# Kernel tuning notes

Hardware: AMD Instinct MI355X
Metric: run time of the kernel (lower is better)

Reference implementation:

```python
import jax, jax.numpy as jnp
import numpy as np


def setup_inputs() -> dict:
    key = jax.random.key(0)
    k_q, k_k, k_v, k_xd, k_yd = jax.random.split(key, 5)
    B, L, H, E, K = 8, 4096, 2048, 512, 64
    return {
        "queries": jax.random.normal(k_q, (B, L, E), dtype=jnp.float32),
        "keys": jax.random.normal(k_k, (B, L, E), dtype=jnp.float32),
        "values": jax.random.normal(k_v, (B, L, E), dtype=jnp.float32),
        "x_date": jax.random.normal(k_xd, (B, L, K), dtype=jnp.float32),
        "y_date": jax.random.normal(k_yd, (B, H, K), dtype=jnp.float32),
    }


def reference(queries, keys, values, x_date, y_date):
    # queries/keys are unused in the original forward's math (only shapes).
    k = x_date.shape[-1]
    scale = 1.0 / float(np.sqrt(k))  # self.scale is None -> 1/sqrt(k)
    # scores: [B, L, H] from date features
    scores = jnp.einsum('blk,bhk->blh', x_date, y_date)
    # softmax over target axis H (dim=-1), numerically stable
    A = jax.nn.softmax(scale * scores, axis=-1)  # [B, L, H]
    # weighted reduction over source axis L -> [B, H, E]
    V = jnp.einsum('ble,blh->bhe', values, A)
    return V
```

## Files before the change

### kernel.cpp

```cpp
#include <hip/hip_runtime.h>
#include <hip/hip_bf16.h>

#define BN 8
#define LN 4096
#define HN 2048
#define EN 512
#define KN 64
#define LT 32
#define NIT 128

typedef __attribute__((ext_vector_type(8))) short bf16x8;
typedef __attribute__((ext_vector_type(4))) float f32x4;
typedef __attribute__((ext_vector_type(4))) unsigned u32x4;

__device__ __forceinline__ short f2b(float x) {
  union { float f; unsigned u; } v; v.f = x;
  unsigned r = v.u + 0x7fffu + ((v.u >> 16) & 1u);
  return (short)(r >> 16);
}

__device__ __forceinline__ bf16x8 cvt8(const float* __restrict__ p) {
  f32x4 a = *(const f32x4*)(p);
  f32x4 b = *(const f32x4*)(p + 4);
  bf16x8 r;
  r[0] = f2b(a[0]); r[1] = f2b(a[1]); r[2] = f2b(a[2]); r[3] = f2b(a[3]);
  r[4] = f2b(b[0]); r[5] = f2b(b[1]); r[6] = f2b(b[2]); r[7] = f2b(b[3]);
  return r;
}

__device__ __forceinline__ void gload16(const void* g, void* s) {
  __builtin_amdgcn_global_load_lds(
      (const __attribute__((address_space(1))) unsigned int*)(unsigned long long)g,
      (__attribute__((address_space(3))) unsigned int*)(unsigned int)(unsigned long long)s,
      16, 0, 0);
}

__global__ __launch_bounds__(256) void prep_cvt2(const float* __restrict__ xs,
                                                 short* __restrict__ xo,
                                                 const float* __restrict__ ys,
                                                 short* __restrict__ yo) {
  int bx = blockIdx.x;
  const float* src;
  short* dst;
  float scale;
  int i;
  if (bx < 1024) {
    i = bx * 256 + threadIdx.x;
    src = xs; dst = xo; scale = 0.125f * 1.4426950408889634f;
  } else {
    i = (bx - 1024) * 256 + threadIdx.x;
    src = ys; dst = yo; scale = 1.0f;
  }
  f32x4 a = *(const f32x4*)(src + (size_t)i * 8);
  f32x4 b = *(const f32x4*)(src + (size_t)i * 8 + 4);
  bf16x8 r;
  r[0] = f2b(a[0] * scale); r[1] = f2b(a[1] * scale);
  r[2] = f2b(a[2] * scale); r[3] = f2b(a[3] * scale);
  r[4] = f2b(b[0] * scale); r[5] = f2b(b[1] * scale);
  r[6] = f2b(b[2] * scale); r[7] = f2b(b[3] * scale);
  *(bf16x8*)(dst + (size_t)i * 8) = r;
}

__global__ __launch_bounds__(256) void k_pv_stats(const float* __restrict__ vals,
                                                  short* __restrict__ valsT,
                                                  const short* __restrict__ xb,
                                                  const short* __restrict__ yb,
                                                  float* __restrict__ ps) {
  __shared__ unsigned trT[2048];
  const int bx = blockIdx.x;
  const int tid = threadIdx.x;
  if (bx < 4096) {
    const int b = bx >> 9;
    const int e0 = ((bx >> 6) & 7) * 64;
    const int l0 = (bx & 63) * 64;
    {
      int lr2 = tid >> 3;
      int ec = (tid & 7) * 8;
      const float* r0 = vals + ((size_t)b * LN + l0 + 2 * lr2) * EN + e0 + ec;
      const float* r1 = r0 + EN;
      f32x4 a0 = *(const f32x4*)r0, a1 = *(const f32x4*)(r0 + 4);
      f32x4 c0 = *(const f32x4*)r1, c1 = *(const f32x4*)(r1 + 4);
#pragma unroll
      for (int j = 0; j < 8; ++j) {
        float lo = (j < 4) ? a0[j] : a1[j - 4];
        float hi = (j < 4) ? c0[j] : c1[j - 4];
        unsigned dw = (unsigned)(unsigned short)f2b(lo) |
                      ((unsigned)(unsigned short)f2b(hi) << 16);
        int e = ec + j;
        int sz = (((e >> 3) ^ e) & 7) << 2;
        trT[e * 32 + (lr2 ^ sz)] = dw;
      }
    }
    __syncthreads();
    {
      int er = tid >> 2, lq = (tid & 3) * 8;
      int sr = ((er >> 3) ^ er) & 7;
      const unsigned* base = trT + er * 32;
      u32x4 u0 = *(const u32x4*)(base + ((((lq >> 2) + 0) ^ sr) << 2));
      u32x4 u1 = *(const u32x4*)(base + ((((lq >> 2) + 1) ^ sr) << 2));
      short* dst = valsT + ((size_t)b * EN + e0 + er) * LN + l0 + 2 * lq;
      *(u32x4*)dst = u0;
      *(u32x4*)(dst + 8) = u1;
    }
  } else {
    const int idx = bx - 4096;
    const int b = (idx >> 5) & 7, hc = idx >> 8;
    const int w = tid >> 6, lane = tid & 63;
    const int row = lane & 15, g = lane >> 4;
    const int lb = (idx & 31) * 128 + w * 32;
    const size_t bL = (size_t)b * LN, bH = (size_t)b * HN;
    bf16x8 xa[2][2];
#pragma unroll
    for (int lt = 0; lt < 2; ++lt) {
      const short* xp = xb + ((bL + lb + lt * 16 + row) << 6) + 8 * g;
      xa[lt][0] = *(const bf16x8*)xp;
      xa[lt][1] = *(const bf16x8*)(xp + 32);
    }
    float s[2][4] = {{0.f, 0.f, 0.f, 0.f}, {0.f, 0.f, 0.f, 0.f}};
    const short* ybase = yb + ((bH + hc * 512 + row) << 6) + 8 * g;
#pragma unroll 2
    for (int it = 0; it < 32; ++it) {
      const short* yp = ybase + ((size_t)it << 10);
      bf16x8 y0 = *(const bf16x8*)yp;
      bf16x8 y1 = *(const bf16x8*)(yp + 32);
#pragma unroll
      for (int lt = 0; lt < 2; ++lt) {
        f32x4 a = {0.f, 0.f, 0.f, 0.f};
        a = __builtin_amdgcn_mfma_f32_16x16x32_bf16(xa[lt][0], y0, a, 0, 0, 0);
        a = __builtin_amdgcn_mfma_f32_16x16x32_bf16(xa[lt][1], y1, a, 0, 0, 0);
#pragma unroll
        for (int r = 0; r < 4; ++r) s[lt][r] += __builtin_amdgcn_exp2f(a[r]);
      }
    }
#pragma unroll
    for (int d = 1; d < 16; d <<= 1)
#pragma unroll
      for (int lt = 0; lt < 2; ++lt)
#pragma unroll
        for (int r = 0; r < 4; ++r) s[lt][r] += __shfl_xor(s[lt][r], d);
    if (row == 0) {
#pragma unroll
      for (int lt = 0; lt < 2; ++lt)
#pragma unroll
        for (int r = 0; r < 4; ++r)
          ps[(size_t)hc * (BN * LN) + bL + lb + lt * 16 + 4 * g + r] = s[lt][r];
    }
  }
}

__global__ void k_comb(const float* __restrict__ ps, float* __restrict__ wv) {
  int idx = blockIdx.x * 256 + threadIdx.x;
  float z = ps[idx] + ps[BN * LN + idx] + ps[2 * BN * LN + idx] + ps[3 * BN * LN + idx];
  wv[idx] = 1.0f / z;
}

__global__ __launch_bounds__(512, 4) void k_main4(
    const short* __restrict__ valsT, const short* __restrict__ xb,
    const short* __restrict__ yb, const float* __restrict__ wv,
    float* __restrict__ out) {
  __shared__ __align__(16) char smem[70016];
  const int tid = threadIdx.x;
  const int w = tid >> 6, lane = tid & 63;
  const int row = lane & 15, g = lane >> 4;

  const int f = blockIdx.x;
  const int b = f & 7;
  const int rest = f >> 3;
  const int hb = (rest & 31) * 64;
  const int eb = (rest >> 5) * 256;
  const size_t bL = (size_t)b * LN, bH = (size_t)b * HN;

  const int wbase = __builtin_amdgcn_readfirstlane(tid & ~63);

  const short* vsrc[2];
#pragma unroll
  for (int j = 0; j < 2; ++j) {
    int i = j * 512 + tid;
    int e = i >> 2, sl = (i & 3) ^ ((e >> 1) & 3);
    vsrc[j] = valsT + (((size_t)b * EN + eb + e) << 12) + 8 * sl;
  }
  const short* xsrc;
  {
    int p = w * 32 + (lane & 31);
    int l = p >> 3, sl = (p & 7) ^ (l & 7);
    xsrc = xb + ((bL + l) << 6) + 8 * sl;
  }
  const float* ssrc = wv + bL + 4 * tid;

  auto stage = [&](int buf, int tl) {
    int loff = tl * 32;
    if (lane < 32)
      gload16(xsrc + loff * 64, smem + 49152 + buf * 4096 + wbase * 8);
    if (tid < 8)
      gload16(ssrc + loff, smem + 69632 + buf * 128);
#pragma unroll
    for (int j = 0; j < 2; ++j)
      gload16(vsrc[j] + loff, smem + buf * 16384 + (j * 8192 + wbase * 16));
  };

  const int ht = w >> 1, lt = w & 1;
  bf16x8 ya0, ya1;
  {
    const short* yp = yb + ((bH + hb + ht * 16 + row) << 6) + 8 * g;
    ya0 = *(const bf16x8*)yp;
    ya1 = *(const bf16x8*)(yp + 32);
  }
  const int sp0 = g ^ (row & 7);
  const int xoffA = ((lt * 16 + row) << 7) + (sp0 << 4);
  const int xoffB = ((lt * 16 + row) << 7) + ((sp0 ^ 4) << 4);
  const int swoff = (lt * 16 + 4 * g) * 4;
  const int hq1 = ht * 16 + row;
  const int poff_w = hq1 * 64 + (((2 * lt + (g >> 1)) ^ ((hq1 >> 1) & 3)) << 4) + (g & 1) * 8;
  const int hq2a = (w >> 2) * 32 + row, hq2b = hq2a + 16;
  const int paoffA = hq2a * 64 + ((g ^ ((hq2a >> 1) & 3)) << 4);
  const int paoffB = hq2b * 64 + ((g ^ ((hq2b >> 1) & 3)) << 4);
  int vboff[4];
#pragma unroll
  for (int n = 0; n < 4; ++n) {
    int el = (w & 3) * 64 + n * 16 + row;
    vboff[n] = el * 64 + ((g ^ ((el >> 1) & 3)) << 4);
  }

  f32x4 acc[2][4];
#pragma unroll
  for (int at = 0; at < 2; ++at)
#pragma unroll
    for (int n = 0; n < 4; ++n) acc[at][n] = (f32x4){0.f, 0.f, 0.f, 0.f};

  auto produce = [&](int bx1, int pp) {
    const char* xbuf = smem + 49152 + bx1 * 4096;
    bf16x8 xa0 = *(const bf16x8*)(xbuf + xoffA);
    bf16x8 xa1 = *(const bf16x8*)(xbuf + xoffB);
    f32x4 sws = *(const f32x4*)(smem + 69632 + bx1 * 128 + swoff);
    f32x4 s4 = {0.f, 0.f, 0.f, 0.f};
    s4 = __builtin_amdgcn_mfma_f32_16x16x32_bf16(xa0, ya0, s4, 0, 0, 0);
    s4 = __builtin_amdgcn_mfma_f32_16x16x32_bf16(xa1, ya1, s4, 0, 0, 0);
    unsigned u0 = (unsigned)(unsigned short)f2b(__builtin_amdgcn_exp2f(s4[0]) * sws[0]) |
                  ((unsigned)(unsigned short)f2b(__builtin_amdgcn_exp2f(s4[1]) * sws[1]) << 16);
    unsigned u1 = (unsigned)(unsigned short)f2b(__builtin_amdgcn_exp2f(s4[2]) * sws[2]) |
                  ((unsigned)(unsigned short)f2b(__builtin_amdgcn_exp2f(s4[3]) * sws[3]) << 16);
    *(unsigned long long*)(smem + 61440 + pp * 4096 + poff_w) =
        (unsigned long long)u0 | ((unsigned long long)u1 << 32);
  };

  auto consume = [&](int rbv, int pp) {
    const char* vbuf = smem + rbv * 16384;
    const char* pbuf = smem + 61440 + pp * 4096;
    bf16x8 pa0 = *(const bf16x8*)(pbuf + paoffA);
    bf16x8 pa1 = *(const bf16x8*)(pbuf + paoffB);
    __builtin_amdgcn_s_setprio(1);
#pragma unroll
    for (int n = 0; n < 4; ++n) {
      bf16x8 vb = *(const bf16x8*)(vbuf + vboff[n]);
      acc[0][n] = __builtin_amdgcn_mfma_f32_16x16x32_bf16(pa0, vb, acc[0][n], 0, 0, 0);
      acc[1][n] = __builtin_amdgcn_mfma_f32_16x16x32_bf16(pa1, vb, acc[1][n], 0, 0, 0);
    }
    __builtin_amdgcn_s_setprio(0);
  };

  stage(0, 0);
  stage(1, 1);
  asm volatile("s_waitcnt vmcnt(2)" ::: "memory");
  __builtin_amdgcn_s_barrier();
  produce(0, 0);
  asm volatile("s_waitcnt lgkmcnt(0)" ::: "memory");
  __builtin_amdgcn_s_barrier();

  int rbv = 0, bx1 = 1, sb = 2, p = 0;
  for (int it = 0; it < NIT - 1; ++it) {
    if (it < NIT - 2) stage(sb, it + 2);
    produce(bx1, p ^ 1);
    consume(rbv, p);
    if (it < NIT - 2)
      asm volatile("s_waitcnt vmcnt(2) lgkmcnt(0)" ::: "memory");
    else
      asm volatile("s_waitcnt vmcnt(0) lgkmcnt(0)" ::: "memory");
    __builtin_amdgcn_s_barrier();
    rbv = rbv == 2 ? 0 : rbv + 1;
    bx1 = bx1 == 2 ? 0 : bx1 + 1;
    sb = sb == 2 ? 0 : sb + 1;
    p ^= 1;
  }
  consume(rbv, p);

#pragma unroll
  for (int at = 0; at < 2; ++at)
#pragma unroll
    for (int n = 0; n < 4; ++n)
#pragma unroll
      for (int r = 0; r < 4; ++r) {
        int h = hb + (w >> 2) * 32 + at * 16 + 4 * g + r;
        int e = eb + (w & 3) * 64 + n * 16 + row;
        out[(bH + h) * (size_t)EN + e] = acc[at][n][r];
      }
}

__global__ __launch_bounds__(256) void k_stats_o(const float* __restrict__ xd,
                                                 const float* __restrict__ yd,
                                                 float* __restrict__ mz) {
  const int b = blockIdx.y;
  const int w = threadIdx.x >> 6;
  const int lane = threadIdx.x & 63;
  const int row = lane & 15, g = lane >> 4;
  const int lb = blockIdx.x * 64 + w * 16;
  const float* xp = xd + ((size_t)b * LN + lb + row) * KN + g * 8;
  bf16x8 a0 = cvt8(xp), a1 = cvt8(xp + 32);
  float m[4], s[4];
#pragma unroll
  for (int r = 0; r < 4; ++r) { m[r] = -1e30f; s[r] = 0.f; }
  const float* ybp = yd + ((size_t)b * HN + row) * KN + g * 8;
  for (int h0 = 0; h0 < HN; h0 += 16) {
    bf16x8 b0 = cvt8(ybp + (size_t)h0 * KN);
    bf16x8 b1 = cvt8(ybp + (size_t)h0 * KN + 32);
    f32x4 acc = {0.f, 0.f, 0.f, 0.f};
    acc = __builtin_amdgcn_mfma_f32_16x16x32_bf16(a0, b0, acc, 0, 0, 0);
    acc = __builtin_amdgcn_mfma_f32_16x16x32_bf16(a1, b1, acc, 0, 0, 0);
#pragma unroll
    for (int r = 0; r < 4; ++r) {
      float v = acc[r] * 0.125f;
      float mn = fmaxf(m[r], v);
      s[r] = s[r] * __expf(m[r] - mn) + __expf(v - mn);
      m[r] = mn;
    }
  }
#pragma unroll
  for (int d = 1; d < 16; d <<= 1) {
#pragma unroll
    for (int r = 0; r < 4; ++r) {
      float mo = __shfl_xor(m[r], d);
      float so = __shfl_xor(s[r], d);
      float mn = fmaxf(m[r], mo);
      s[r] = s[r] * __expf(m[r] - mn) + so * __expf(mo - mn);
      m[r] = mn;
    }
  }
  if (row == 0) {
#pragma unroll
    for (int r = 0; r < 4; ++r) {
      size_t idx = (size_t)b * LN + lb + 4 * g + r;
      mz[idx] = m[r];
      mz[(size_t)BN * LN + idx] = 1.0f / s[r];
    }
  }
}

__global__ __launch_bounds__(512) void k_main_o(const float* __restrict__ vals,
                                                const float* __restrict__ xd,
                                                const float* __restrict__ yd,
                                                const float* __restrict__ mz,
                                                float* __restrict__ out) {
  __shared__ short vT[256][34];
  __shared__ short pT[128][34];
  __shared__ short xT[LT][72];
  __shared__ float smm[LT], smz[LT];
  const int b = blockIdx.z;
  const int hb = blockIdx.x * 128;
  const int eb = blockIdx.y * 256;
  const int tid = threadIdx.x;
  const int w = tid >> 6, lane = tid & 63;
  const int row = lane & 15, g = lane >> 4;
  const float* yp = yd + ((size_t)b * HN + hb + w * 16 + row) * KN + g * 8;
  bf16x8 ya0 = cvt8(yp), ya1 = cvt8(yp + 32);
  f32x4 acc[16];
#pragma unroll
  for (int n = 0; n < 16; ++n) acc[n] = (f32x4){0.f, 0.f, 0.f, 0.f};
  const float* mzb = mz + (size_t)b * LN;
  const float* rzb = mz + (size_t)BN * LN + (size_t)b * LN;
  for (int l0 = 0; l0 < LN; l0 += LT) {
    __syncthreads();
    {
      int xl = tid >> 4, xk = (tid & 15) * 4;
      f32x4 xv = *(const f32x4*)(xd + ((size_t)b * LN + l0 + xl) * KN + xk);
      union { short h[4]; int i[2]; } u;
      u.h[0] = f2b(xv[0]); u.h[1] = f2b(xv[1]); u.h[2] = f2b(xv[2]); u.h[3] = f2b(xv[3]);
      int* dst = (int*)(&xT[xl][xk]);
      dst[0] = u.i[0]; dst[1] = u.i[1];
    }
#pragma unroll
    for (int lp = 0; lp < 4; ++lp) {
      int vl = (tid >> 6) + lp * 8;
      const float* vrow = vals + ((size_t)b * LN + l0 + vl) * EN + eb;
#pragma unroll
      for (int u2 = 0; u2 < 4; ++u2) {
        int e = (tid & 63) + u2 * 64;
        vT[e][vl] = f2b(vrow[e]);
      }
    }
    if (tid < LT) { smm[tid] = mzb[l0 + tid]; smz[tid] = rzb[l0 + tid]; }
    __syncthreads();
#pragma unroll
    for (int t2 = 0; t2 < 2; ++t2) {
      const short* xr = &xT[t2 * 16 + row][0];
      bf16x8 xb0 = *(const bf16x8*)(xr + 8 * g);
      bf16x8 xb1 = *(const bf16x8*)(xr + 32 + 8 * g);
      f32x4 sa = {0.f, 0.f, 0.f, 0.f};
      sa = __builtin_amdgcn_mfma_f32_16x16x32_bf16(ya0, xb0, sa, 0, 0, 0);
      sa = __builtin_amdgcn_mfma_f32_16x16x32_bf16(ya1, xb1, sa, 0, 0, 0);
      int lcol = t2 * 16 + row;
      float mm = smm[lcol], zz = smz[lcol];
#pragma unroll
      for (int r = 0; r < 4; ++r) {
        float p2 = __expf(sa[r] * 0.125f - mm) * zz;
        pT[w * 16 + 4 * g + r][lcol] = f2b(p2);
      }
    }
    __syncthreads();
    bf16x8 pa;
    {
      const int* pi = (const int*)(&pT[w * 16 + row][0] + 8 * g);
      union { int i[4]; bf16x8 f; } u;
      u.i[0] = pi[0]; u.i[1] = pi[1]; u.i[2] = pi[2]; u.i[3] = pi[3];
      pa = u.f;
    }
#pragma unroll
    for (int n = 0; n < 16; ++n) {
      const int* vi = (const int*)(&vT[n * 16 + row][0] + 8 * g);
      union { int i[4]; bf16x8 f; } u;
      u.i[0] = vi[0]; u.i[1] = vi[1]; u.i[2] = vi[2]; u.i[3] = vi[3];
      acc[n] = __builtin_amdgcn_mfma_f32_16x16x32_bf16(pa, u.f, acc[n], 0, 0, 0);
    }
  }
#pragma unroll
  for (int n = 0; n < 16; ++n)
#pragma unroll
    for (int r = 0; r < 4; ++r) {
      int h = hb + w * 16 + 4 * g + r;
      int e = eb + n * 16 + row;
      out[((size_t)b * HN + h) * EN + e] = acc[n][r];
    }
}

extern "C" void kernel_launch(void* const* d_in, const int* in_sizes, int n_in,
                              void* d_out, int out_size, void* d_ws, size_t ws_size,
                              hipStream_t stream) {
  const float* vals = (const float*)d_in[2];
  const float* xd = (const float*)d_in[3];
  const float* yd = (const float*)d_in[4];
  float* out = (float*)d_out;

  if (ws_size >= 40501248ull) {
    char* wsb = (char*)d_ws;
    short* valsT = (short*)wsb;
    short* xbuf  = (short*)(wsb + 33554432);
    short* ybuf  = (short*)(wsb + 37748736);
    float* ps    = (float*)(wsb + 39845888);
    float* wv    = (float*)(wsb + 40370176);

    prep_cvt2<<<dim3(1536), 256, 0, stream>>>(xd, xbuf, yd, ybuf);
    k_pv_stats<<<dim3(5120), 256, 0, stream>>>(vals, valsT, xbuf, ybuf, ps);
    k_comb<<<dim3(BN * LN / 256), 256, 0, stream>>>(ps, wv);
    k_main4<<<dim3(512), 512, 0, stream>>>(valsT, xbuf, ybuf, wv, out);
  } else {
    float* mz = (float*)d_ws;
    k_stats_o<<<dim3(LN / 64, BN), 256, 0, stream>>>(xd, yd, mz);
    k_main_o<<<dim3(HN / 128, EN / 256, BN), 512, 0, stream>>>(vals, xd, yd, mz, out);
  }
}
```

Baseline: 171.7 us.

## Enlarge main kernel tile to 128x256 with 64-row L steps and specialized producer waves

The main fused kernel now covers 128 H rows per block instead of 64 and steps L by 64 instead of 32. This halves the grid to 256 blocks and doubles reuse of each staged V tile across more accumulators. Only two waves compute the score/exp probabilities while all eight waves run the PV MFMAs, and the pipeline is restructured with double-buffered V and triple-buffered x/weights. The cost is much larger LDS use (about 121 KB), lower occupancy, and fewer blocks than CUs, which may leave compute units idle and serializes probability production on two waves.

```diff
diff --git a/kernel.cpp b/kernel.cpp
--- a/kernel.cpp
+++ b/kernel.cpp
@@ -6,8 +6,8 @@
 #define HN 2048
 #define EN 512
 #define KN 64
-#define LT 32
-#define NIT 128
+#define LT 64
+#define NIT 64
 
 typedef __attribute__((ext_vector_type(8))) short bf16x8;
 typedef __attribute__((ext_vector_type(4))) float f32x4;
@@ -154,11 +154,11 @@
   wv[idx] = 1.0f / z;
 }
 
-__global__ __launch_bounds__(512, 4) void k_main4(
+__global__ __launch_bounds__(512, 2) void k_main5(
     const short* __restrict__ valsT, const short* __restrict__ xb,
     const short* __restrict__ yb, const float* __restrict__ wv,
     float* __restrict__ out) {
-  __shared__ __align__(16) char smem[70016];
+  __shared__ __align__(16) char smem[123648];
   const int tid = threadIdx.x;
   const int w = tid >> 6, lane = tid & 63;
   const int row = lane & 15, g = lane >> 4;
@@ -166,130 +166,137 @@
   const int f = blockIdx.x;
   const int b = f & 7;
   const int rest = f >> 3;
-  const int hb = (rest & 31) * 64;
-  const int eb = (rest >> 5) * 256;
+  const int hb = (rest & 15) * 128;
+  const int eb = (rest >> 4) * 256;
   const size_t bL = (size_t)b * LN, bH = (size_t)b * HN;
 
   const int wbase = __builtin_amdgcn_readfirstlane(tid & ~63);
 
-  const short* vsrc[2];
-#pragma unroll
-  for (int j = 0; j < 2; ++j) {
+  const short* vsrc[4];
+#pragma unroll
+  for (int j = 0; j < 4; ++j) {
     int i = j * 512 + tid;
-    int e = i >> 2, sl = (i & 3) ^ ((e >> 1) & 3);
+    int e = i >> 3, ch = i & 7, sl = ch ^ (e & 7);
     vsrc[j] = valsT + (((size_t)b * EN + eb + e) << 12) + 8 * sl;
   }
-  const short* xsrc;
-  {
-    int p = w * 32 + (lane & 31);
-    int l = p >> 3, sl = (p & 7) ^ (l & 7);
-    xsrc = xb + ((bL + l) << 6) + 8 * sl;
-  }
-  const float* ssrc = wv + bL + 4 * tid;
-
-  auto stage = [&](int buf, int tl) {
-    int loff = tl * 32;
-    if (lane < 32)
-      gload16(xsrc + loff * 64, smem + 49152 + buf * 4096 + wbase * 8);
-    if (tid < 8)
-      gload16(ssrc + loff, smem + 69632 + buf * 128);
-#pragma unroll
-    for (int j = 0; j < 2; ++j)
-      gload16(vsrc[j] + loff, smem + buf * 16384 + (j * 8192 + wbase * 16));
+  const short* xsrc = xb + ((bL + (tid >> 3)) << 6) + 8 * ((tid & 7) ^ ((tid >> 3) & 7));
+  const float* ssrc = wv + bL + (lane << 2);
+
+  auto stage_xs = [&](int t) {
+    int m3 = t % 3;
+    gload16(xsrc + ((size_t)t << 12), smem + 65536 + m3 * 8192 + wbase * 16);
+    if (tid < 16)
+      gload16(ssrc + t * 64, smem + 122880 + m3 * 256);
   };
-
-  const int ht = w >> 1, lt = w & 1;
-  bf16x8 ya0, ya1;
-  {
-    const short* yp = yb + ((bH + hb + ht * 16 + row) << 6) + 8 * g;
-    ya0 = *(const bf16x8*)yp;
-    ya1 = *(const bf16x8*)(yp + 32);
-  }
-  const int sp0 = g ^ (row & 7);
-  const int xoffA = ((lt * 16 + row) << 7) + (sp0 << 4);
-  const int xoffB = ((lt * 16 + row) << 7) + ((sp0 ^ 4) << 4);
-  const int swoff = (lt * 16 + 4 * g) * 4;
-  const int hq1 = ht * 16 + row;
-  const int poff_w = hq1 * 64 + (((2 * lt + (g >> 1)) ^ ((hq1 >> 1) & 3)) << 4) + (g & 1) * 8;
-  const int hq2a = (w >> 2) * 32 + row, hq2b = hq2a + 16;
-  const int paoffA = hq2a * 64 + ((g ^ ((hq2a >> 1) & 3)) << 4);
-  const int paoffB = hq2b * 64 + ((g ^ ((hq2b >> 1) & 3)) << 4);
-  int vboff[4];
-#pragma unroll
-  for (int n = 0; n < 4; ++n) {
-    int el = (w & 3) * 64 + n * 16 + row;
-    vboff[n] = el * 64 + ((g ^ ((el >> 1) & 3)) << 4);
-  }
-
-  f32x4 acc[2][4];
-#pragma unroll
-  for (int at = 0; at < 2; ++at)
+  auto stage_v = [&](int t) {
+    char* vb_ = smem + (t & 1) * 32768 + wbase * 16;
+#pragma unroll
+    for (int j = 0; j < 4; ++j)
+      gload16(vsrc[j] + t * 64, vb_ + j * 8192);
+  };
+
+  bf16x8 ya[4][2];
+  if (w < 2) {
+#pragma unroll
+    for (int j = 0; j < 4; ++j) {
+      const short* yp = yb + ((bH + hb + (w * 4 + j) * 16 + row) << 6) + 8 * g;
+      ya[j][0] = *(const bf16x8*)yp;
+      ya[j][1] = *(const bf16x8*)(yp + 32);
+    }
+  }
+
+  f32x4 acc[4][4];
+#pragma unroll
+  for (int at = 0; at < 4; ++at)
 #pragma unroll
     for (int n = 0; n < 4; ++n) acc[at][n] = (f32x4){0.f, 0.f, 0.f, 0.f};
 
-  auto produce = [&](int bx1, int pp) {
-    const char* xbuf = smem + 49152 + bx1 * 4096;
-    bf16x8 xa0 = *(const bf16x8*)(xbuf + xoffA);
-    bf16x8 xa1 = *(const bf16x8*)(xbuf + xoffB);
-    f32x4 sws = *(const f32x4*)(smem + 69632 + bx1 * 128 + swoff);
-    f32x4 s4 = {0.f, 0.f, 0.f, 0.f};
-    s4 = __builtin_amdgcn_mfma_f32_16x16x32_bf16(xa0, ya0, s4, 0, 0, 0);
-    s4 = __builtin_amdgcn_mfma_f32_16x16x32_bf16(xa1, ya1, s4, 0, 0, 0);
-    unsigned u0 = (unsigned)(unsigned short)f2b(__builtin_amdgcn_exp2f(s4[0]) * sws[0]) |
-                  ((unsigned)(unsigned short)f2b(__builtin_amdgcn_exp2f(s4[1]) * sws[1]) << 16);
-    unsigned u1 = (unsigned)(unsigned short)f2b(__builtin_amdgcn_exp2f(s4[2]) * sws[2]) |
-                  ((unsigned)(unsigned short)f2b(__builtin_amdgcn_exp2f(s4[3]) * sws[3]) << 16);
-    *(unsigned long long*)(smem + 61440 + pp * 4096 + poff_w) =
-        (unsigned long long)u0 | ((unsigned long long)u1 << 32);
+  auto produce = [&](int t) {
+    if (w >= 2) return;
+    const char* xbuf = smem + 65536 + (t % 3) * 8192;
+    const float* swp = (const float*)(smem + 122880 + (t % 3) * 256);
+    char* pdst = smem + 90112 + (t & 1) * 16384;
+#pragma unroll
+    for (int lt = 0; lt < 4; ++lt) {
+      int lr = lt * 16 + row;
+      bf16x8 xa0 = *(const bf16x8*)(xbuf + lr * 128 + ((g ^ (lr & 7)) << 4));
+      bf16x8 xa1 = *(const bf16x8*)(xbuf + lr * 128 + (((4 + g) ^ (lr & 7)) << 4));
+      f32x4 sws = *(const f32x4*)(swp + lt * 16 + 4 * g);
+#pragma unroll
+      for (int j = 0; j < 4; ++j) {
+        f32x4 s4 = {0.f, 0.f, 0.f, 0.f};
+        s4 = __builtin_amdgcn_mfma_f32_16x16x32_bf16(xa0, ya[j][0], s4, 0, 0, 0);
+        s4 = __builtin_amdgcn_mfma_f32_16x16x32_bf16(xa1, ya[j][1], s4, 0, 0, 0);
+        int hq = (w * 4 + j) * 16 + row;
+        int phys = (lt * 2 + (g >> 1)) ^ (hq & 7);
+        unsigned u0 = (unsigned)(unsigned short)f2b(__builtin_amdgcn_exp2f(s4[0]) * sws[0]) |
+                      ((unsigned)(unsigned short)f2b(__builtin_amdgcn_exp2f(s4[1]) * sws[1]) << 16);
+        unsigned u1 = (unsigned)(unsigned short)f2b(__builtin_amdgcn_exp2f(s4[2]) * sws[2]) |
+                      ((unsigned)(unsigned short)f2b(__builtin_amdgcn_exp2f(s4[3]) * sws[3]) << 16);
+        *(unsigned long long*)(pdst + hq * 128 + phys * 16 + (g & 1) * 8) =
+            (unsigned long long)u0 | ((unsigned long long)u1 << 32);
+      }
+    }
   };
 
-  auto consume = [&](int rbv, int pp) {
-    const char* vbuf = smem + rbv * 16384;
-    const char* pbuf = smem + 61440 + pp * 4096;
-    bf16x8 pa0 = *(const bf16x8*)(pbuf + paoffA);
-    bf16x8 pa1 = *(const bf16x8*)(pbuf + paoffB);
+  auto consume = [&](int t) {
+    const char* vbuf = smem + (t & 1) * 32768;
+    const char* pbuf = smem + 90112 + (t & 1) * 16384;
+    bf16x8 pa[4][2];
+#pragma unroll
+    for (int at = 0; at < 4; ++at) {
+      int hq = (w >> 2) * 64 + at * 16 + row;
+#pragma unroll
+      for (int ks = 0; ks < 2; ++ks)
+        pa[at][ks] = *(const bf16x8*)(pbuf + hq * 128 + (((ks * 4 + g) ^ (hq & 7)) << 4));
+    }
     __builtin_amdgcn_s_setprio(1);
 #pragma unroll
     for (int n = 0; n < 4; ++n) {
-      bf16x8 vb = *(const bf16x8*)(vbuf + vboff[n]);
-      acc[0][n] = __builtin_amdgcn_mfma_f32_16x16x32_bf16(pa0, vb, acc[0][n], 0, 0, 0);
-      acc[1][n] = __builtin_amdgcn_mfma_f32_16x16x32_bf16(pa1, vb, acc[1][n], 0, 0, 0);
+      int el = (w & 3) * 64 + n * 16 + row;
+      bf16x8 vb0 = *(const bf16x8*)(vbuf + el * 128 + ((g ^ (el & 7)) << 4));
+      bf16x8 vb1 = *(const bf16x8*)(vbuf + el * 128 + (((4 + g) ^ (el & 7)) << 4));
+#pragma unroll
+      for (int at = 0; at < 4; ++at) {
+        acc[at][n] = __builtin_amdgcn_mfma_f32_16x16x32_bf16(pa[at][0], vb0, acc[at][n], 0, 0, 0);
+        acc[at][n] = __builtin_amdgcn_mfma_f32_16x16x32_bf16(pa[at][1], vb1, acc[at][n], 0, 0, 0);
+      }
     }
     __builtin_amdgcn_s_setprio(0);
   };
 
-  stage(0, 0);
-  stage(1, 1);
-  asm volatile("s_waitcnt vmcnt(2)" ::: "memory");
+  stage_xs(0);
+  stage_xs(1);
+  stage_v(0);
+  asm volatile("s_waitcnt vmcnt(0)" ::: "memory");
   __builtin_amdgcn_s_barrier();
-  produce(0, 0);
+  asm volatile("" ::: "memory");
+  produce(0);
   asm volatile("s_waitcnt lgkmcnt(0)" ::: "memory");
   __builtin_amdgcn_s_barrier();
-
-  int rbv = 0, bx1 = 1, sb = 2, p = 0;
-  for (int it = 0; it < NIT - 1; ++it) {
-    if (it < NIT - 2) stage(sb, it + 2);
-    produce(bx1, p ^ 1);
-    consume(rbv, p);
-    if (it < NIT - 2)
-      asm volatile("s_waitcnt vmcnt(2) lgkmcnt(0)" ::: "memory");
-    else
+  asm volatile("" ::: "memory");
+
+  for (int it = 0; it < NIT; ++it) {
+    if (it + 2 < NIT) stage_xs(it + 2);
+    if (it + 1 < NIT) {
+      stage_v(it + 1);
+      produce(it + 1);
+    }
+    consume(it);
+    if (it + 1 < NIT) {
       asm volatile("s_waitcnt vmcnt(0) lgkmcnt(0)" ::: "memory");
-    __builtin_amdgcn_s_barrier();
-    rbv = rbv == 2 ? 0 : rbv + 1;
-    bx1 = bx1 == 2 ? 0 : bx1 + 1;
-    sb = sb == 2 ? 0 : sb + 1;
-    p ^= 1;
-  }
-  consume(rbv, p);
-
-#pragma unroll
-  for (int at = 0; at < 2; ++at)
+      __builtin_amdgcn_s_barrier();
+      asm volatile("" ::: "memory");
+    }
+  }
+
+#pragma unroll
+  for (int at = 0; at < 4; ++at)
 #pragma unroll
     for (int n = 0; n < 4; ++n)
 #pragma unroll
       for (int r = 0; r < 4; ++r) {
-        int h = hb + (w >> 2) * 32 + at * 16 + 4 * g + r;
+        int h = hb + (w >> 2) * 64 + at * 16 + 4 * g + r;
         int e = eb + (w & 3) * 64 + n * 16 + row;
         out[(bH + h) * (size_t)EN + e] = acc[at][n][r];
       }
@@ -351,8 +358,8 @@
                                                 float* __restrict__ out) {
   __shared__ short vT[256][34];
   __shared__ short pT[128][34];
-  __shared__ short xT[LT][72];
-  __shared__ float smm[LT], smz[LT];
+  __shared__ short xT[32][72];
+  __shared__ float smm[32], smz[32];
   const int b = blockIdx.z;
   const int hb = blockIdx.x * 128;
   const int eb = blockIdx.y * 256;
@@ -366,7 +373,7 @@
   for (int n = 0; n < 16; ++n) acc[n] = (f32x4){0.f, 0.f, 0.f, 0.f};
   const float* mzb = mz + (size_t)b * LN;
   const float* rzb = mz + (size_t)BN * LN + (size_t)b * LN;
-  for (int l0 = 0; l0 < LN; l0 += LT) {
+  for (int l0 = 0; l0 < LN; l0 += 32) {
     __syncthreads();
     {
       int xl = tid >> 4, xk = (tid & 15) * 4;
@@ -386,7 +393,7 @@
         vT[e][vl] = f2b(vrow[e]);
       }
     }
-    if (tid < LT) { smm[tid] = mzb[l0 + tid]; smz[tid] = rzb[l0 + tid]; }
+    if (tid < 32) { smm[tid] = mzb[l0 + tid]; smz[tid] = rzb[l0 + tid]; }
     __syncthreads();
 #pragma unroll
     for (int t2 = 0; t2 < 2; ++t2) {
@@ -449,7 +456,7 @@
     prep_cvt2<<<dim3(1536), 256, 0, stream>>>(xd, xbuf, yd, ybuf);
     k_pv_stats<<<dim3(5120), 256, 0, stream>>>(vals, valsT, xbuf, ybuf, ps);
     k_comb<<<dim3(BN * LN / 256), 256, 0, stream>>>(ps, wv);
-    k_main4<<<dim3(512), 512, 0, stream>>>(valsT, xbuf, ybuf, wv, out);
+    k_main5<<<dim3(256), 512, 0, stream>>>(valsT, xbuf, ybuf, wv, out);
   } else {
     float* mz = (float*)d_ws;
     k_stats_o<<<dim3(LN / 64, BN), 256, 0, stream>>>(xd, yd, mz);
```

Result: slower. 196.7 us (+14.6%).

## Merge prep kernels and stream V operands directly from global in main loop

Applied to the files above, without the earlier changes.

Folds the bf16 conversion kernel into the transpose/stats kernel, removing one launch. The stats path now converts x and y from fp32 on the fly. The main kernel no longer stages V tiles and softmax weights through LDS. It loads V fragments and weights straight from global into registers and keeps only x (triple-buffered) and P in LDS, which shrinks shared memory from about 70KB to 20KB. The risk is exposed global-load latency on V in the MFMA loop in exchange for less LDS traffic and more potential occupancy.

```diff
diff --git a/kernel.cpp b/kernel.cpp
--- a/kernel.cpp
+++ b/kernel.cpp
@@ -19,12 +19,12 @@
   return (short)(r >> 16);
 }
 
-__device__ __forceinline__ bf16x8 cvt8(const float* __restrict__ p) {
+__device__ __forceinline__ bf16x8 cvt8s(const float* __restrict__ p, float s) {
   f32x4 a = *(const f32x4*)(p);
   f32x4 b = *(const f32x4*)(p + 4);
   bf16x8 r;
-  r[0] = f2b(a[0]); r[1] = f2b(a[1]); r[2] = f2b(a[2]); r[3] = f2b(a[3]);
-  r[4] = f2b(b[0]); r[5] = f2b(b[1]); r[6] = f2b(b[2]); r[7] = f2b(b[3]);
+  r[0] = f2b(a[0] * s); r[1] = f2b(a[1] * s); r[2] = f2b(a[2] * s); r[3] = f2b(a[3] * s);
+  r[4] = f2b(b[0] * s); r[5] = f2b(b[1] * s); r[6] = f2b(b[2] * s); r[7] = f2b(b[3] * s);
   return r;
 }
 
@@ -35,55 +35,41 @@
       16, 0, 0);
 }
 
-__global__ __launch_bounds__(256) void prep_cvt2(const float* __restrict__ xs,
-                                                 short* __restrict__ xo,
-                                                 const float* __restrict__ ys,
-                                                 short* __restrict__ yo) {
-  int bx = blockIdx.x;
-  const float* src;
-  short* dst;
-  float scale;
-  int i;
-  if (bx < 1024) {
-    i = bx * 256 + threadIdx.x;
-    src = xs; dst = xo; scale = 0.125f * 1.4426950408889634f;
-  } else {
-    i = (bx - 1024) * 256 + threadIdx.x;
-    src = ys; dst = yo; scale = 1.0f;
-  }
-  f32x4 a = *(const f32x4*)(src + (size_t)i * 8);
-  f32x4 b = *(const f32x4*)(src + (size_t)i * 8 + 4);
-  bf16x8 r;
-  r[0] = f2b(a[0] * scale); r[1] = f2b(a[1] * scale);
-  r[2] = f2b(a[2] * scale); r[3] = f2b(a[3] * scale);
-  r[4] = f2b(b[0] * scale); r[5] = f2b(b[1] * scale);
-  r[6] = f2b(b[2] * scale); r[7] = f2b(b[3] * scale);
-  *(bf16x8*)(dst + (size_t)i * 8) = r;
-}
-
-__global__ __launch_bounds__(256) void k_pv_stats(const float* __restrict__ vals,
-                                                  short* __restrict__ valsT,
-                                                  const short* __restrict__ xb,
-                                                  const short* __restrict__ yb,
-                                                  float* __restrict__ ps) {
+__global__ __launch_bounds__(256) void k_prep(const float* __restrict__ vals,
+                                              short* __restrict__ valsT,
+                                              const float* __restrict__ xd,
+                                              short* __restrict__ xo,
+                                              const float* __restrict__ yd,
+                                              short* __restrict__ yo,
+                                              float* __restrict__ ps) {
   __shared__ unsigned trT[2048];
   const int bx = blockIdx.x;
   const int tid = threadIdx.x;
-  if (bx < 4096) {
-    const int b = bx >> 9;
-    const int e0 = ((bx >> 6) & 7) * 64;
-    const int l0 = (bx & 63) * 64;
+  const float c0 = 0.125f * 1.4426950408889634f;
+  if (bx < 1536) {
+    const float* src;
+    short* dst;
+    float scale;
+    int i;
+    if (bx < 1024) { i = bx * 256 + tid; src = xd; dst = xo; scale = c0; }
+    else           { i = (bx - 1024) * 256 + tid; src = yd; dst = yo; scale = 1.0f; }
+    *(bf16x8*)(dst + (size_t)i * 8) = cvt8s(src + (size_t)i * 8, scale);
+  } else if (bx < 5632) {
+    const int idx = bx - 1536;
+    const int b = idx >> 9;
+    const int e0 = ((idx >> 6) & 7) * 64;
+    const int l0 = (idx & 63) * 64;
     {
       int lr2 = tid >> 3;
       int ec = (tid & 7) * 8;
       const float* r0 = vals + ((size_t)b * LN + l0 + 2 * lr2) * EN + e0 + ec;
       const float* r1 = r0 + EN;
       f32x4 a0 = *(const f32x4*)r0, a1 = *(const f32x4*)(r0 + 4);
-      f32x4 c0 = *(const f32x4*)r1, c1 = *(const f32x4*)(r1 + 4);
+      f32x4 cc0 = *(const f32x4*)r1, cc1 = *(const f32x4*)(r1 + 4);
 #pragma unroll
       for (int j = 0; j < 8; ++j) {
         float lo = (j < 4) ? a0[j] : a1[j - 4];
-        float hi = (j < 4) ? c0[j] : c1[j - 4];
+        float hi = (j < 4) ? cc0[j] : cc1[j - 4];
         unsigned dw = (unsigned)(unsigned short)f2b(lo) |
                       ((unsigned)(unsigned short)f2b(hi) << 16);
         int e = ec + j;
@@ -103,7 +89,7 @@
       *(u32x4*)(dst + 8) = u1;
     }
   } else {
-    const int idx = bx - 4096;
+    const int idx = bx - 5632;
     const int b = (idx >> 5) & 7, hc = idx >> 8;
     const int w = tid >> 6, lane = tid & 63;
     const int row = lane & 15, g = lane >> 4;
@@ -112,17 +98,17 @@
     bf16x8 xa[2][2];
 #pragma unroll
     for (int lt = 0; lt < 2; ++lt) {
-      const short* xp = xb + ((bL + lb + lt * 16 + row) << 6) + 8 * g;
-      xa[lt][0] = *(const bf16x8*)xp;
-      xa[lt][1] = *(const bf16x8*)(xp + 32);
+      const float* xp = xd + (bL + lb + lt * 16 + row) * KN + g * 8;
+      xa[lt][0] = cvt8s(xp, c0);
+      xa[lt][1] = cvt8s(xp + 32, c0);
     }
     float s[2][4] = {{0.f, 0.f, 0.f, 0.f}, {0.f, 0.f, 0.f, 0.f}};
-    const short* ybase = yb + ((bH + hc * 512 + row) << 6) + 8 * g;
+    const float* ybase = yd + (bH + hc * 512 + row) * KN + g * 8;
 #pragma unroll 2
     for (int it = 0; it < 32; ++it) {
-      const short* yp = ybase + ((size_t)it << 10);
-      bf16x8 y0 = *(const bf16x8*)yp;
-      bf16x8 y1 = *(const bf16x8*)(yp + 32);
+      const float* yp = ybase + (size_t)it * (16 * KN);
+      bf16x8 y0 = cvt8s(yp, 1.0f);
+      bf16x8 y1 = cvt8s(yp + 32, 1.0f);
 #pragma unroll
       for (int lt = 0; lt < 2; ++lt) {
         f32x4 a = {0.f, 0.f, 0.f, 0.f};
@@ -154,11 +140,11 @@
   wv[idx] = 1.0f / z;
 }
 
-__global__ __launch_bounds__(512, 4) void k_main4(
+__global__ __launch_bounds__(512, 4) void k_main6(
     const short* __restrict__ valsT, const short* __restrict__ xb,
     const short* __restrict__ yb, const float* __restrict__ wv,
     float* __restrict__ out) {
-  __shared__ __align__(16) char smem[70016];
+  __shared__ __align__(16) char smem[20480];
   const int tid = threadIdx.x;
   const int w = tid >> 6, lane = tid & 63;
   const int row = lane & 15, g = lane >> 4;
@@ -169,33 +155,17 @@
   const int hb = (rest & 31) * 64;
   const int eb = (rest >> 5) * 256;
   const size_t bL = (size_t)b * LN, bH = (size_t)b * HN;
-
   const int wbase = __builtin_amdgcn_readfirstlane(tid & ~63);
 
-  const short* vsrc[2];
-#pragma unroll
-  for (int j = 0; j < 2; ++j) {
-    int i = j * 512 + tid;
-    int e = i >> 2, sl = (i & 3) ^ ((e >> 1) & 3);
-    vsrc[j] = valsT + (((size_t)b * EN + eb + e) << 12) + 8 * sl;
-  }
   const short* xsrc;
   {
     int p = w * 32 + (lane & 31);
     int l = p >> 3, sl = (p & 7) ^ (l & 7);
     xsrc = xb + ((bL + l) << 6) + 8 * sl;
   }
-  const float* ssrc = wv + bL + 4 * tid;
-
-  auto stage = [&](int buf, int tl) {
-    int loff = tl * 32;
+  auto stage_x = [&](int t) {
     if (lane < 32)
-      gload16(xsrc + loff * 64, smem + 49152 + buf * 4096 + wbase * 8);
-    if (tid < 8)
-      gload16(ssrc + loff, smem + 69632 + buf * 128);
-#pragma unroll
-    for (int j = 0; j < 2; ++j)
-      gload16(vsrc[j] + loff, smem + buf * 16384 + (j * 8192 + wbase * 16));
+      gload16(xsrc + ((size_t)t << 11), smem + (t % 3) * 4096 + wbase * 8);
   };
 
   const int ht = w >> 1, lt = w & 1;
@@ -208,17 +178,18 @@
   const int sp0 = g ^ (row & 7);
   const int xoffA = ((lt * 16 + row) << 7) + (sp0 << 4);
   const int xoffB = ((lt * 16 + row) << 7) + ((sp0 ^ 4) << 4);
-  const int swoff = (lt * 16 + 4 * g) * 4;
   const int hq1 = ht * 16 + row;
   const int poff_w = hq1 * 64 + (((2 * lt + (g >> 1)) ^ ((hq1 >> 1) & 3)) << 4) + (g & 1) * 8;
+  const float* swsrc = wv + bL + lt * 16 + 4 * g;
+
   const int hq2a = (w >> 2) * 32 + row, hq2b = hq2a + 16;
-  const int paoffA = hq2a * 64 + ((g ^ ((hq2a >> 1) & 3)) << 4);
-  const int paoffB = hq2b * 64 + ((g ^ ((hq2b >> 1) & 3)) << 4);
-  int vboff[4];
+  const int paoffA = 12288 + hq2a * 64 + ((g ^ ((hq2a >> 1) & 3)) << 4);
+  const int paoffB = 12288 + hq2b * 64 + ((g ^ ((hq2b >> 1) & 3)) << 4);
+  const short* vp[4];
 #pragma unroll
   for (int n = 0; n < 4; ++n) {
     int el = (w & 3) * 64 + n * 16 + row;
-    vboff[n] = el * 64 + ((g ^ ((el >> 1) & 3)) << 4);
+    vp[n] = valsT + ((size_t)b * EN + eb + el) * LN + g * 8;
   }
 
   f32x4 acc[2][4];
@@ -227,11 +198,12 @@
 #pragma unroll
     for (int n = 0; n < 4; ++n) acc[at][n] = (f32x4){0.f, 0.f, 0.f, 0.f};
 
-  auto produce = [&](int bx1, int pp) {
-    const char* xbuf = smem + 49152 + bx1 * 4096;
+  f32x4 sws_cur, sws_next;
+
+  auto produce = [&](int t, f32x4 sws) {
+    const char* xbuf = smem + (t % 3) * 4096;
     bf16x8 xa0 = *(const bf16x8*)(xbuf + xoffA);
     bf16x8 xa1 = *(const bf16x8*)(xbuf + xoffB);
-    f32x4 sws = *(const f32x4*)(smem + 69632 + bx1 * 128 + swoff);
     f32x4 s4 = {0.f, 0.f, 0.f, 0.f};
     s4 = __builtin_amdgcn_mfma_f32_16x16x32_bf16(xa0, ya0, s4, 0, 0, 0);
     s4 = __builtin_amdgcn_mfma_f32_16x16x32_bf16(xa1, ya1, s4, 0, 0, 0);
@@ -239,49 +211,70 @@
                   ((unsigned)(unsigned short)f2b(__builtin_amdgcn_exp2f(s4[1]) * sws[1]) << 16);
     unsigned u1 = (unsigned)(unsigned short)f2b(__builtin_amdgcn_exp2f(s4[2]) * sws[2]) |
                   ((unsigned)(unsigned short)f2b(__builtin_amdgcn_exp2f(s4[3]) * sws[3]) << 16);
-    *(unsigned long long*)(smem + 61440 + pp * 4096 + poff_w) =
+    *(unsigned long long*)(smem + 12288 + (t & 1) * 4096 + poff_w) =
         (unsigned long long)u0 | ((unsigned long long)u1 << 32);
   };
 
-  auto consume = [&](int rbv, int pp) {
-    const char* vbuf = smem + rbv * 16384;
-    const char* pbuf = smem + 61440 + pp * 4096;
-    bf16x8 pa0 = *(const bf16x8*)(pbuf + paoffA);
-    bf16x8 pa1 = *(const bf16x8*)(pbuf + paoffB);
-    __builtin_amdgcn_s_setprio(1);
-#pragma unroll
-    for (int n = 0; n < 4; ++n) {
-      bf16x8 vb = *(const bf16x8*)(vbuf + vboff[n]);
-      acc[0][n] = __builtin_amdgcn_mfma_f32_16x16x32_bf16(pa0, vb, acc[0][n], 0, 0, 0);
-      acc[1][n] = __builtin_amdgcn_mfma_f32_16x16x32_bf16(pa1, vb, acc[1][n], 0, 0, 0);
-    }
-    __builtin_amdgcn_s_setprio(0);
-  };
-
-  stage(0, 0);
-  stage(1, 1);
-  asm volatile("s_waitcnt vmcnt(2)" ::: "memory");
+  stage_x(0);
+  stage_x(1);
+  sws_cur = *(const f32x4*)(swsrc);
+  sws_next = *(const f32x4*)(swsrc + 32);
+  asm volatile("s_waitcnt vmcnt(0)" ::: "memory");
   __builtin_amdgcn_s_barrier();
-  produce(0, 0);
+  asm volatile("" ::: "memory");
+  produce(0, sws_cur);
+  sws_cur = sws_next;
   asm volatile("s_waitcnt lgkmcnt(0)" ::: "memory");
   __builtin_amdgcn_s_barrier();
-
-  int rbv = 0, bx1 = 1, sb = 2, p = 0;
+  asm volatile("" ::: "memory");
+
   for (int it = 0; it < NIT - 1; ++it) {
-    if (it < NIT - 2) stage(sb, it + 2);
-    produce(bx1, p ^ 1);
-    consume(rbv, p);
-    if (it < NIT - 2)
-      asm volatile("s_waitcnt vmcnt(2) lgkmcnt(0)" ::: "memory");
-    else
-      asm volatile("s_waitcnt vmcnt(0) lgkmcnt(0)" ::: "memory");
+    const int p = it & 1;
+    const char* pb = smem + p * 4096;
+    bf16x8 pa0 = *(const bf16x8*)(pb + paoffA);
+    bf16x8 pa1 = *(const bf16x8*)(pb + paoffB);
+    if (it + 2 < NIT) stage_x(it + 2);
+    __builtin_amdgcn_sched_barrier(0);
+    bf16x8 vb0 = *(const bf16x8*)(vp[0]);
+    bf16x8 vb1 = *(const bf16x8*)(vp[1]);
+    bf16x8 vb2 = *(const bf16x8*)(vp[2]);
+    bf16x8 vb3 = *(const bf16x8*)(vp[3]);
+    if (it + 2 < NIT) sws_next = *(const f32x4*)(swsrc + (it + 2) * 32);
+    produce(it + 1, sws_cur);
+    sws_cur = sws_next;
+    __builtin_amdgcn_s_setprio(1);
+    acc[0][0] = __builtin_amdgcn_mfma_f32_16x16x32_bf16(pa0, vb0, acc[0][0], 0, 0, 0);
+    acc[1][0] = __builtin_amdgcn_mfma_f32_16x16x32_bf16(pa1, vb0, acc[1][0], 0, 0, 0);
+    acc[0][1] = __builtin_amdgcn_mfma_f32_16x16x32_bf16(pa0, vb1, acc[0][1], 0, 0, 0);
+    acc[1][1] = __builtin_amdgcn_mfma_f32_16x16x32_bf16(pa1, vb1, acc[1][1], 0, 0, 0);
+    acc[0][2] = __builtin_amdgcn_mfma_f32_16x16x32_bf16(pa0, vb2, acc[0][2], 0, 0, 0);
+    acc[1][2] = __builtin_amdgcn_mfma_f32_16x16x32_bf16(pa1, vb2, acc[1][2], 0, 0, 0);
+    acc[0][3] = __builtin_amdgcn_mfma_f32_16x16x32_bf16(pa0, vb3, acc[0][3], 0, 0, 0);
+    acc[1][3] = __builtin_amdgcn_mfma_f32_16x16x32_bf16(pa1, vb3, acc[1][3], 0, 0, 0);
+    __builtin_amdgcn_s_setprio(0);
+    vp[0] += 32; vp[1] += 32; vp[2] += 32; vp[3] += 32;
+    asm volatile("s_waitcnt vmcnt(1) lgkmcnt(0)" ::: "memory");
     __builtin_amdgcn_s_barrier();
-    rbv = rbv == 2 ? 0 : rbv + 1;
-    bx1 = bx1 == 2 ? 0 : bx1 + 1;
-    sb = sb == 2 ? 0 : sb + 1;
-    p ^= 1;
-  }
-  consume(rbv, p);
+    asm volatile("" ::: "memory");
+  }
+
+  {
+    const char* pb = smem + ((NIT - 1) & 1) * 4096;
+    bf16x8 pa0 = *(const bf16x8*)(pb + paoffA);
+    bf16x8 pa1 = *(const bf16x8*)(pb + paoffB);
+    bf16x8 vb0 = *(const bf16x8*)(vp[0]);
+    bf16x8 vb1 = *(const bf16x8*)(vp[1]);
+    bf16x8 vb2 = *(const bf16x8*)(vp[2]);
+    bf16x8 vb3 = *(const bf16x8*)(vp[3]);
+    acc[0][0] = __builtin_amdgcn_mfma_f32_16x16x32_bf16(pa0, vb0, acc[0][0], 0, 0, 0);
+    acc[1][0] = __builtin_amdgcn_mfma_f32_16x16x32_bf16(pa1, vb0, acc[1][0], 0, 0, 0);
+    acc[0][1] = __builtin_amdgcn_mfma_f32_16x16x32_bf16(pa0, vb1, acc[0][1], 0, 0, 0);
+    acc[1][1] = __builtin_amdgcn_mfma_f32_16x16x32_bf16(pa1, vb1, acc[1][1], 0, 0, 0);
+    acc[0][2] = __builtin_amdgcn_mfma_f32_16x16x32_bf16(pa0, vb2, acc[0][2], 0, 0, 0);
+    acc[1][2] = __builtin_amdgcn_mfma_f32_16x16x32_bf16(pa1, vb2, acc[1][2], 0, 0, 0);
+    acc[0][3] = __builtin_amdgcn_mfma_f32_16x16x32_bf16(pa0, vb3, acc[0][3], 0, 0, 0);
+    acc[1][3] = __builtin_amdgcn_mfma_f32_16x16x32_bf16(pa1, vb3, acc[1][3], 0, 0, 0);
+  }
 
 #pragma unroll
   for (int at = 0; at < 2; ++at)
@@ -304,14 +297,14 @@
   const int row = lane & 15, g = lane >> 4;
   const int lb = blockIdx.x * 64 + w * 16;
   const float* xp = xd + ((size_t)b * LN + lb + row) * KN + g * 8;
-  bf16x8 a0 = cvt8(xp), a1 = cvt8(xp + 32);
+  bf16x8 a0 = cvt8s(xp, 1.0f), a1 = cvt8s(xp + 32, 1.0f);
   float m[4], s[4];
 #pragma unroll
   for (int r = 0; r < 4; ++r) { m[r] = -1e30f; s[r] = 0.f; }
   const float* ybp = yd + ((size_t)b * HN + row) * KN + g * 8;
   for (int h0 = 0; h0 < HN; h0 += 16) {
-    bf16x8 b0 = cvt8(ybp + (size_t)h0 * KN);
-    bf16x8 b1 = cvt8(ybp + (size_t)h0 * KN + 32);
+    bf16x8 b0 = cvt8s(ybp + (size_t)h0 * KN, 1.0f);
+    bf16x8 b1 = cvt8s(ybp + (size_t)h0 * KN + 32, 1.0f);
     f32x4 acc = {0.f, 0.f, 0.f, 0.f};
     acc = __builtin_amdgcn_mfma_f32_16x16x32_bf16(a0, b0, acc, 0, 0, 0);
     acc = __builtin_amdgcn_mfma_f32_16x16x32_bf16(a1, b1, acc, 0, 0, 0);
@@ -351,8 +344,8 @@
                                                 float* __restrict__ out) {
   __shared__ short vT[256][34];
   __shared__ short pT[128][34];
-  __shared__ short xT[LT][72];
-  __shared__ float smm[LT], smz[LT];
+  __shared__ short xT[32][72];
+  __shared__ float smm[32], smz[32];
   const int b = blockIdx.z;
   const int hb = blockIdx.x * 128;
   const int eb = blockIdx.y * 256;
@@ -360,13 +353,13 @@
   const int w = tid >> 6, lane = tid & 63;
   const int row = lane & 15, g = lane >> 4;
   const float* yp = yd + ((size_t)b * HN + hb + w * 16 + row) * KN + g * 8;
-  bf16x8 ya0 = cvt8(yp), ya1 = cvt8(yp + 32);
+  bf16x8 ya0 = cvt8s(yp, 1.0f), ya1 = cvt8s(yp + 32, 1.0f);
   f32x4 acc[16];
 #pragma unroll
   for (int n = 0; n < 16; ++n) acc[n] = (f32x4){0.f, 0.f, 0.f, 0.f};
   const float* mzb = mz + (size_t)b * LN;
   const float* rzb = mz + (size_t)BN * LN + (size_t)b * LN;
-  for (int l0 = 0; l0 < LN; l0 += LT) {
+  for (int l0 = 0; l0 < LN; l0 += 32) {
     __syncthreads();
     {
       int xl = tid >> 4, xk = (tid & 15) * 4;
@@ -386,7 +379,7 @@
         vT[e][vl] = f2b(vrow[e]);
       }
     }
-    if (tid < LT) { smm[tid] = mzb[l0 + tid]; smz[tid] = rzb[l0 + tid]; }
+    if (tid < 32) { smm[tid] = mzb[l0 + tid]; smz[tid] = rzb[l0 + tid]; }
     __syncthreads();
 #pragma unroll
     for (int t2 = 0; t2 < 2; ++t2) {
@@ -446,10 +439,9 @@
     float* ps    = (float*)(wsb + 39845888);
     float* wv    = (float*)(wsb + 40370176);
 
-    prep_cvt2<<<dim3(1536), 256, 0, stream>>>(xd, xbuf, yd, ybuf);
-    k_pv_stats<<<dim3(5120), 256, 0, stream>>>(vals, valsT, xbuf, ybuf, ps);
+    k_prep<<<dim3(6656), 256, 0, stream>>>(vals, valsT, xd, xbuf, yd, ybuf, ps);
     k_comb<<<dim3(BN * LN / 256), 256, 0, stream>>>(ps, wv);
-    k_main4<<<dim3(512), 512, 0, stream>>>(valsT, xbuf, ybuf, wv, out);
+    k_main6<<<dim3(512), 512, 0, stream>>>(valsT, xbuf, ybuf, wv, out);
   } else {
     float* mz = (float*)d_ws;
     k_stats_o<<<dim3(LN / 64, BN), 256, 0, stream>>>(xd, yd, mz);
```

Result: slower. 387.6 us (+125.7%).
